# Kernel optimization log

Measured on AMD Instinct MI355X. Metric: run time of the kernel, lower is better.

The kernel has to match this reference:

```python
import jax, jax.numpy as jnp
import numpy as np

N = 40000
C_IN, C_OUT = 64, 128
SHAPE = (512, 16, 512)   # (x, height, z); dim=1 -> n_kernels=16
BEV_H, BEV_W = 512, 512  # bev_dims = [0, 2]
N_KERNELS = 16
BATCH = 2


def setup_inputs() -> dict:
    key = jax.random.key(0)
    k1, k2, k3, k4, k5, k6 = jax.random.split(key, 6)
    x = jax.random.randint(k1, (N,), 0, BEV_H, dtype=jnp.int32)
    h = jax.random.randint(k2, (N,), 0, N_KERNELS, dtype=jnp.int32)
    z = jax.random.randint(k3, (N,), 0, BEV_W, dtype=jnp.int32)
    b = jax.random.randint(k4, (N,), 0, BATCH, dtype=jnp.int32)
    coords = jnp.stack([x, h, z, b], axis=1)  # [N, 4]
    feats = jax.random.normal(k5, (N, C_IN), dtype=jnp.float32)
    std = 1.0 / np.sqrt(C_IN)
    kernel = jax.random.uniform(k6, (N_KERNELS, C_IN, C_OUT), dtype=jnp.float32,
                                minval=-std, maxval=std)
    return {"coords": coords, "feats": feats, "kernel": kernel,
            "stride": 1, "batch_size": BATCH}


def reference(coords, feats, kernel, stride, batch_size):
    # gather per-point kernel by height bin (dim=1), offset is zero
    kidx = coords[:, 1] // stride                      # [N]
    per_point_k = kernel[kidx]                         # [N, C_in, C_out]
    f = jnp.einsum('nc,nco->no', feats, per_point_k)   # [N, C_out]
    # flat BEV index: batch * (H*W) + x * W + z
    b = coords[:, 3].astype(jnp.int32)
    xb = (coords[:, 0] // stride).astype(jnp.int32)
    zb = (coords[:, 2] // stride).astype(jnp.int32)
    idx = b * (BEV_H * BEV_W) + xb * BEV_W + zb        # [N]
    num_seg = batch_size * BEV_H * BEV_W
    dense = jax.ops.segment_sum(f, idx, num_segments=num_seg)  # [B*H*W, C_out]
    out = dense.reshape(batch_size, BEV_H, BEV_W, C_OUT)
    return jnp.transpose(out, (0, 3, 1, 2))            # [B, C_out, H, W]
```

## Files before the change

### kernel.cpp

```cpp
#include <hip/hip_runtime.h>


#define CIN    64
#define COUT   128
#define BEVH   512
#define BEVW   512
#define HW     (BEVH * BEVW)
#define NBINS  16
#define PTS_PER_WAVE  8
#define PTS_PER_BLOCK 32

__global__ __launch_bounds__(256) void bev_sort(
    const int* __restrict__ coords,
    const int* __restrict__ stride_p,
    int*       __restrict__ gcnt,
    int*       __restrict__ sorted,
    int n)
{
    __shared__ int hist[NBINS];
    __shared__ int base[NBINS];
    const int tid = threadIdx.x;
    if (tid < NBINS) hist[tid] = 0;
    __syncthreads();

    const int i = blockIdx.x * 256 + tid;
    int k = 0, rank = 0;
    if (i < n) {
        k = coords[i * 4 + 1] / stride_p[0];
        rank = atomicAdd(&hist[k], 1);
    }
    __syncthreads();
    if (tid < NBINS)
        base[tid] = hist[tid] ? atomicAdd(&gcnt[tid], hist[tid]) : 0;
    __syncthreads();
    if (i < n)
        sorted[k * n + base[k] + rank] = i;
}

__global__ __launch_bounds__(256) void bev_point(
    const int*   __restrict__ coords,
    const float* __restrict__ feats,
    const float* __restrict__ kern,
    const int*   __restrict__ stride_p,
    const int*   __restrict__ gcnt,
    const int*   __restrict__ sorted,
    float*       __restrict__ f,
    int*         __restrict__ head,
    int*         __restrict__ nxt,
    int n, int chunks_per_bin)
{
    __shared__ float lk[CIN * COUT];

    const int bin   = blockIdx.x / chunks_per_bin;
    const int chunk = blockIdx.x % chunks_per_bin;
    const int cnt   = gcnt[bin];
    const int r0blk = chunk * PTS_PER_BLOCK;
    if (r0blk >= cnt) return;

    {
        const float4* src = (const float4*)(kern + (size_t)bin * CIN * COUT);
        float4* dst = (float4*)lk;
#pragma unroll
        for (int j = 0; j < 8; ++j)
            dst[j * 256 + threadIdx.x] = src[j * 256 + threadIdx.x];
    }
    __syncthreads();

    const int wave = threadIdx.x >> 6;
    const int lane = threadIdx.x & 63;
    const int r0 = r0blk + wave * PTS_PER_WAVE;
    const int navail = cnt - r0;
    if (navail <= 0) return;
    const int np = navail < PTS_PER_WAVE ? navail : PTS_PER_WAVE;

    int pts[PTS_PER_WAVE];
#pragma unroll
    for (int p = 0; p < PTS_PER_WAVE; ++p) {
        const int rr = (p < np) ? (r0 + p) : r0;
        pts[p] = __builtin_amdgcn_readfirstlane(sorted[bin * n + rr]);
    }

    float ax[PTS_PER_WAVE], ay[PTS_PER_WAVE];
#pragma unroll
    for (int p = 0; p < PTS_PER_WAVE; ++p) { ax[p] = 0.f; ay[p] = 0.f; }

#pragma unroll
    for (int c = 0; c < CIN; ++c) {
        const float2 kv = *(const float2*)&lk[c * COUT + 2 * lane];
#pragma unroll
        for (int p = 0; p < PTS_PER_WAVE; ++p) {
            const float fv = feats[(size_t)pts[p] * CIN + c];
            ax[p] = fmaf(fv, kv.x, ax[p]);
            ay[p] = fmaf(fv, kv.y, ay[p]);
        }
    }

#pragma unroll
    for (int p = 0; p < PTS_PER_WAVE; ++p) {
        if (p < np)
            *(float2*)(f + (size_t)pts[p] * COUT + 2 * lane) = make_float2(ax[p], ay[p]);
    }

    if (lane == 0) {
        const int stride = stride_p[0];
        for (int p = 0; p < np; ++p) {
            const int pt = pts[p];
            const int cx = coords[pt * 4 + 0];
            const int cz = coords[pt * 4 + 2];
            const int cb = coords[pt * 4 + 3];
            const int cell = (cb << 18) + ((cx / stride) << 9) + (cz / stride);
            const int old = atomicExch(&head[cell], pt + 1);
            nxt[pt] = old;
        }
    }
}

__global__ __launch_bounds__(256) void bev_accum(
    const int* __restrict__ coords,
    const int* __restrict__ stride_p,
    float*     __restrict__ f,
    const int* __restrict__ head,
    const int* __restrict__ nxt,
    int n)
{
    const int wave = threadIdx.x >> 6;
    const int lane = threadIdx.x & 63;
    int pt = blockIdx.x * 4 + wave;
    if (pt >= n) return;
    pt = __builtin_amdgcn_readfirstlane(pt);

    const int nx0 = __builtin_amdgcn_readfirstlane(nxt[pt]);
    if (nx0 == 0) return;

    const int stride = stride_p[0];
    const int cx = coords[pt * 4 + 0];
    const int cz = coords[pt * 4 + 2];
    const int cb = coords[pt * 4 + 3];
    const int cell = (cb << 18) + ((cx / stride) << 9) + (cz / stride);
    if (__builtin_amdgcn_readfirstlane(head[cell]) != pt + 1) return;

    float2 acc = *(const float2*)(f + (size_t)pt * COUT + 2 * lane);
    int p = nx0;
    while (p) {
        const float2 v = *(const float2*)(f + (size_t)(p - 1) * COUT + 2 * lane);
        acc.x += v.x; acc.y += v.y;
        p = __builtin_amdgcn_readfirstlane(nxt[p - 1]);
    }
    *(float2*)(f + (size_t)pt * COUT + 2 * lane) = acc;
}

__global__ __launch_bounds__(256) void bev_dense_row(
    const float* __restrict__ f,
    const int*   __restrict__ head,
    float*       __restrict__ out,
    int nrows)
{
    const int wave = threadIdx.x >> 6;
    const int lane = threadIdx.x & 63;
    const int row = blockIdx.x * 4 + wave;
    if (row >= nrows) return;

    const int x = row & 511;
    const int o = (row >> 9) & 127;
    const int b = row >> 16;
    const int* hrow = head + (b << 18) + (x << 9);
    float* const orow = out + (size_t)row * 512;

#pragma unroll
    for (int h = 0; h < 2; ++h) {
        const int z = h * 256 + lane * 4;
        const int4 h4 = *(const int4*)(hrow + z);
        float4 v = make_float4(0.f, 0.f, 0.f, 0.f);
        if (h4.x) v.x = f[(size_t)(h4.x - 1) * COUT + o];
        if (h4.y) v.y = f[(size_t)(h4.y - 1) * COUT + o];
        if (h4.z) v.z = f[(size_t)(h4.z - 1) * COUT + o];
        if (h4.w) v.w = f[(size_t)(h4.w - 1) * COUT + o];
        *(float4*)(orow + z) = v;
    }
}

extern "C" void kernel_launch(void* const* d_in, const int* in_sizes, int n_in,
                              void* d_out, int out_size, void* d_ws, size_t ws_size,
                              hipStream_t stream) {
    const int*   coords   = (const int*)d_in[0];
    const float* feats    = (const float*)d_in[1];
    const float* kern     = (const float*)d_in[2];
    const int*   stride_p = (const int*)d_in[3];
    float* out = (float*)d_out;

    const int n      = in_sizes[0] / 4;
    const int ncells = out_size / COUT;

    size_t off = 0;
    float* f = (float*)((char*)d_ws + off);          off += (size_t)n * COUT * sizeof(float);
    int* head = (int*)((char*)d_ws + off);           off += (size_t)ncells * sizeof(int);
    int* gcnt = (int*)((char*)d_ws + off);           off += NBINS * sizeof(int);
    int* nxt  = (int*)((char*)d_ws + off);           off += (size_t)n * sizeof(int);
    int* sorted = (int*)((char*)d_ws + off);         off += (size_t)NBINS * n * sizeof(int);

    (void)hipMemsetAsync(head, 0,
                         (size_t)ncells * sizeof(int) + NBINS * sizeof(int), stream);

    bev_sort<<<(n + 255) / 256, 256, 0, stream>>>(coords, stride_p, gcnt, sorted, n);

    const int chunks_per_bin = (n + PTS_PER_BLOCK - 1) / PTS_PER_BLOCK;
    bev_point<<<NBINS * chunks_per_bin, 256, 0, stream>>>(
        coords, feats, kern, stride_p, gcnt, sorted, f, head, nxt,
        n, chunks_per_bin);

    bev_accum<<<(n + 3) / 4, 256, 0, stream>>>(coords, stride_p, f, head, nxt, n);

    const int nrows = out_size / 512;
    bev_dense_row<<<nrows / 4, 256, 0, stream>>>(f, head, out, nrows);
}
```

Measured before the change: 349.2 us.

## Fuse head zeroing into sort, compact point grid, fold accumulation into dense pass

Removes the memset by zeroing the head table inside the sort kernel, and replaces global bin counters with per-block histograms that each point block prefix-scans to place its points. The launch grid shrinks from one block per chunk per bin to the number of non-empty chunks. The separate linked-list accumulation kernel is dropped; the dense output kernel now walks each cell's list directly. The trade-off is a redundant histogram reduction and scan in every point block, and repeated list walks per output channel. Zeroing head in the sort kernel is only safe because the later kernels run after it on the stream.

```diff
diff --git a/kernel.cpp b/kernel.cpp
--- a/kernel.cpp
+++ b/kernel.cpp
@@ -13,62 +13,108 @@
 __global__ __launch_bounds__(256) void bev_sort(
     const int* __restrict__ coords,
     const int* __restrict__ stride_p,
-    int*       __restrict__ gcnt,
+    int*       __restrict__ head,
+    int*       __restrict__ blkhist,
     int*       __restrict__ sorted,
-    int n)
+    int n, int nblk, int scap, int ncells)
 {
     __shared__ int hist[NBINS];
-    __shared__ int base[NBINS];
     const int tid = threadIdx.x;
+    const int vb  = blockIdx.x;
+
+    {
+        int4* h4 = (int4*)head;
+        const int tot4 = ncells >> 2;
+        const int zero_stride = nblk * 256;
+        for (int i = vb * 256 + tid; i < tot4; i += zero_stride)
+            h4[i] = make_int4(0, 0, 0, 0);
+    }
+
     if (tid < NBINS) hist[tid] = 0;
     __syncthreads();
 
-    const int i = blockIdx.x * 256 + tid;
+    const int i = vb * 256 + tid;
     int k = 0, rank = 0;
     if (i < n) {
         k = coords[i * 4 + 1] / stride_p[0];
         rank = atomicAdd(&hist[k], 1);
     }
     __syncthreads();
+    if (i < n)
+        sorted[k * scap + vb * 256 + rank] = i;
     if (tid < NBINS)
-        base[tid] = hist[tid] ? atomicAdd(&gcnt[tid], hist[tid]) : 0;
-    __syncthreads();
-    if (i < n)
-        sorted[k * n + base[k] + rank] = i;
-}
-
-__global__ __launch_bounds__(256) void bev_point(
+        blkhist[vb * NBINS + tid] = hist[tid];
+}
+
+__global__ __launch_bounds__(256, 4) void bev_point(
     const int*   __restrict__ coords,
     const float* __restrict__ feats,
     const float* __restrict__ kern,
     const int*   __restrict__ stride_p,
-    const int*   __restrict__ gcnt,
+    const int*   __restrict__ blkhist,
     const int*   __restrict__ sorted,
     float*       __restrict__ f,
     int*         __restrict__ head,
     int*         __restrict__ nxt,
-    int n, int chunks_per_bin)
+    int n, int nblk, int scap)
 {
     __shared__ float lk[CIN * COUT];
-
-    const int bin   = blockIdx.x / chunks_per_bin;
-    const int chunk = blockIdx.x % chunks_per_bin;
-    const int cnt   = gcnt[bin];
-    const int r0blk = chunk * PTS_PER_BLOCK;
-    if (r0blk >= cnt) return;
+    __shared__ int sc[256];
+    __shared__ int tot[NBINS];
+    __shared__ int cbase[NBINS + 1];
+
+    const int tid = threadIdx.x;
+
+    if (tid < NBINS) tot[tid] = 0;
+    __syncthreads();
+    if (tid < nblk) {
+#pragma unroll
+        for (int k = 0; k < NBINS; ++k)
+            atomicAdd(&tot[k], blkhist[tid * NBINS + k]);
+    }
+    __syncthreads();
+    if (tid == 0) {
+        int acc = 0;
+        cbase[0] = 0;
+        for (int k = 0; k < NBINS; ++k) {
+            acc += (tot[k] + PTS_PER_BLOCK - 1) / PTS_PER_BLOCK;
+            cbase[k + 1] = acc;
+        }
+    }
+    __syncthreads();
+
+    const int c = blockIdx.x;
+    if (c >= cbase[NBINS]) return;
+
+    int bin = 0;
+    while (cbase[bin + 1] <= c) ++bin;
+    const int chunk = c - cbase[bin];
+    const int cnt   = tot[bin];
+
+    {
+        int v = (tid < nblk) ? blkhist[tid * NBINS + bin] : 0;
+        sc[tid] = v;
+        __syncthreads();
+        for (int off = 1; off < 256; off <<= 1) {
+            const int add = (tid >= off) ? sc[tid - off] : 0;
+            __syncthreads();
+            sc[tid] += add;
+            __syncthreads();
+        }
+    }
 
     {
         const float4* src = (const float4*)(kern + (size_t)bin * CIN * COUT);
         float4* dst = (float4*)lk;
 #pragma unroll
         for (int j = 0; j < 8; ++j)
-            dst[j * 256 + threadIdx.x] = src[j * 256 + threadIdx.x];
-    }
-    __syncthreads();
-
-    const int wave = threadIdx.x >> 6;
-    const int lane = threadIdx.x & 63;
-    const int r0 = r0blk + wave * PTS_PER_WAVE;
+            dst[j * 256 + tid] = src[j * 256 + tid];
+    }
+    __syncthreads();
+
+    const int wave = tid >> 6;
+    const int lane = tid & 63;
+    const int r0 = chunk * PTS_PER_BLOCK + wave * PTS_PER_WAVE;
     const int navail = cnt - r0;
     if (navail <= 0) return;
     const int np = navail < PTS_PER_WAVE ? navail : PTS_PER_WAVE;
@@ -77,7 +123,13 @@
 #pragma unroll
     for (int p = 0; p < PTS_PER_WAVE; ++p) {
         const int rr = (p < np) ? (r0 + p) : r0;
-        pts[p] = __builtin_amdgcn_readfirstlane(sorted[bin * n + rr]);
+        int lo = 0, hi = nblk;
+        while (lo < hi) {
+            const int mid = (lo + hi) >> 1;
+            if (sc[mid] > rr) hi = mid; else lo = mid + 1;
+        }
+        const int local = rr - (lo ? sc[lo - 1] : 0);
+        pts[p] = __builtin_amdgcn_readfirstlane(sorted[bin * scap + lo * 256 + local]);
     }
 
     float ax[PTS_PER_WAVE], ay[PTS_PER_WAVE];
@@ -85,11 +137,11 @@
     for (int p = 0; p < PTS_PER_WAVE; ++p) { ax[p] = 0.f; ay[p] = 0.f; }
 
 #pragma unroll
-    for (int c = 0; c < CIN; ++c) {
-        const float2 kv = *(const float2*)&lk[c * COUT + 2 * lane];
+    for (int cc = 0; cc < CIN; ++cc) {
+        const float2 kv = *(const float2*)&lk[cc * COUT + 2 * lane];
 #pragma unroll
         for (int p = 0; p < PTS_PER_WAVE; ++p) {
-            const float fv = feats[(size_t)pts[p] * CIN + c];
+            const float fv = feats[(size_t)pts[p] * CIN + cc];
             ax[p] = fmaf(fv, kv.x, ax[p]);
             ay[p] = fmaf(fv, kv.y, ay[p]);
         }
@@ -115,43 +167,10 @@
     }
 }
 
-__global__ __launch_bounds__(256) void bev_accum(
-    const int* __restrict__ coords,
-    const int* __restrict__ stride_p,
-    float*     __restrict__ f,
-    const int* __restrict__ head,
-    const int* __restrict__ nxt,
-    int n)
-{
-    const int wave = threadIdx.x >> 6;
-    const int lane = threadIdx.x & 63;
-    int pt = blockIdx.x * 4 + wave;
-    if (pt >= n) return;
-    pt = __builtin_amdgcn_readfirstlane(pt);
-
-    const int nx0 = __builtin_amdgcn_readfirstlane(nxt[pt]);
-    if (nx0 == 0) return;
-
-    const int stride = stride_p[0];
-    const int cx = coords[pt * 4 + 0];
-    const int cz = coords[pt * 4 + 2];
-    const int cb = coords[pt * 4 + 3];
-    const int cell = (cb << 18) + ((cx / stride) << 9) + (cz / stride);
-    if (__builtin_amdgcn_readfirstlane(head[cell]) != pt + 1) return;
-
-    float2 acc = *(const float2*)(f + (size_t)pt * COUT + 2 * lane);
-    int p = nx0;
-    while (p) {
-        const float2 v = *(const float2*)(f + (size_t)(p - 1) * COUT + 2 * lane);
-        acc.x += v.x; acc.y += v.y;
-        p = __builtin_amdgcn_readfirstlane(nxt[p - 1]);
-    }
-    *(float2*)(f + (size_t)pt * COUT + 2 * lane) = acc;
-}
-
 __global__ __launch_bounds__(256) void bev_dense_row(
     const float* __restrict__ f,
     const int*   __restrict__ head,
+    const int*   __restrict__ nxt,
     float*       __restrict__ out,
     int nrows)
 {
@@ -171,10 +190,17 @@
         const int z = h * 256 + lane * 4;
         const int4 h4 = *(const int4*)(hrow + z);
         float4 v = make_float4(0.f, 0.f, 0.f, 0.f);
-        if (h4.x) v.x = f[(size_t)(h4.x - 1) * COUT + o];
-        if (h4.y) v.y = f[(size_t)(h4.y - 1) * COUT + o];
-        if (h4.z) v.z = f[(size_t)(h4.z - 1) * COUT + o];
-        if (h4.w) v.w = f[(size_t)(h4.w - 1) * COUT + o];
+        int p0 = h4.x, p1 = h4.y, p2 = h4.z, p3 = h4.w;
+        if (p0) { v.x = f[(size_t)(p0 - 1) * COUT + o]; p0 = nxt[p0 - 1]; }
+        if (p1) { v.y = f[(size_t)(p1 - 1) * COUT + o]; p1 = nxt[p1 - 1]; }
+        if (p2) { v.z = f[(size_t)(p2 - 1) * COUT + o]; p2 = nxt[p2 - 1]; }
+        if (p3) { v.w = f[(size_t)(p3 - 1) * COUT + o]; p3 = nxt[p3 - 1]; }
+        while (p0 | p1 | p2 | p3) {
+            if (p0) { v.x += f[(size_t)(p0 - 1) * COUT + o]; p0 = nxt[p0 - 1]; }
+            if (p1) { v.y += f[(size_t)(p1 - 1) * COUT + o]; p1 = nxt[p1 - 1]; }
+            if (p2) { v.z += f[(size_t)(p2 - 1) * COUT + o]; p2 = nxt[p2 - 1]; }
+            if (p3) { v.w += f[(size_t)(p3 - 1) * COUT + o]; p3 = nxt[p3 - 1]; }
+        }
         *(float4*)(orow + z) = v;
     }
 }
@@ -190,26 +216,24 @@
 
     const int n      = in_sizes[0] / 4;
     const int ncells = out_size / COUT;
+    const int nblk   = (n + 255) / 256;
+    const int scap   = nblk * 256;
 
     size_t off = 0;
-    float* f = (float*)((char*)d_ws + off);          off += (size_t)n * COUT * sizeof(float);
-    int* head = (int*)((char*)d_ws + off);           off += (size_t)ncells * sizeof(int);
-    int* gcnt = (int*)((char*)d_ws + off);           off += NBINS * sizeof(int);
-    int* nxt  = (int*)((char*)d_ws + off);           off += (size_t)n * sizeof(int);
-    int* sorted = (int*)((char*)d_ws + off);         off += (size_t)NBINS * n * sizeof(int);
-
-    (void)hipMemsetAsync(head, 0,
-                         (size_t)ncells * sizeof(int) + NBINS * sizeof(int), stream);
-
-    bev_sort<<<(n + 255) / 256, 256, 0, stream>>>(coords, stride_p, gcnt, sorted, n);
-
-    const int chunks_per_bin = (n + PTS_PER_BLOCK - 1) / PTS_PER_BLOCK;
-    bev_point<<<NBINS * chunks_per_bin, 256, 0, stream>>>(
-        coords, feats, kern, stride_p, gcnt, sorted, f, head, nxt,
-        n, chunks_per_bin);
-
-    bev_accum<<<(n + 3) / 4, 256, 0, stream>>>(coords, stride_p, f, head, nxt, n);
+    float* f      = (float*)((char*)d_ws + off); off += (size_t)n * COUT * sizeof(float);
+    int* head     = (int*)((char*)d_ws + off);   off += (size_t)ncells * sizeof(int);
+    int* nxt      = (int*)((char*)d_ws + off);   off += (size_t)n * sizeof(int);
+    int* blkhist  = (int*)((char*)d_ws + off);   off += (size_t)nblk * NBINS * sizeof(int);
+    int* sorted   = (int*)((char*)d_ws + off);   off += (size_t)NBINS * scap * sizeof(int);
+
+    bev_sort<<<nblk, 256, 0, stream>>>(coords, stride_p, head, blkhist, sorted,
+                                       n, nblk, scap, ncells);
+
+    const int max_chunks = (n + PTS_PER_BLOCK - 1) / PTS_PER_BLOCK + NBINS;
+    bev_point<<<max_chunks, 256, 0, stream>>>(coords, feats, kern, stride_p,
+                                              blkhist, sorted, f, head, nxt,
+                                              n, nblk, scap);
 
     const int nrows = out_size / 512;
-    bev_dense_row<<<nrows / 4, 256, 0, stream>>>(f, head, out, nrows);
-}
+    bev_dense_row<<<nrows / 4, 256, 0, stream>>>(f, head, nxt, out, nrows);
+}
```

After: 450.9 us. 29.1% more time.
